# Optimization experiments

Measured on AMD Instinct MI355X. Metric: run time of the kernel, lower is better.

## Reference

```python
import jax, jax.numpy as jnp
import numpy as np

B = 1024          # batch of positions
K = 64            # king squares
F = 640           # 64 squares * 10 piece types
C = 256           # accumulator channels


def setup_inputs() -> dict:
    key = jax.random.key(0)
    k1, k2, k3 = jax.random.split(key, 3)
    piece_positions = jax.random.randint(k1, (B, 64, 10), 0, 2).astype(jnp.bool_)
    king_positions = jax.random.randint(k2, (B, 2), 0, K, dtype=jnp.int32)
    input_weights = jax.random.normal(k3, (K, F + 1, C), dtype=jnp.float32)
    bias = jnp.zeros((C,), dtype=jnp.float32)
    return {
        "piece_positions": piece_positions,
        "king_positions": king_positions,
        "input_weights": input_weights,
        "bias": bias,
    }


def reference(piece_positions, king_positions, input_weights, bias):
    # Flatten the (64, 10) boolean piece plane into 640 HalfKP features.
    b = piece_positions.shape[0]
    p = piece_positions.reshape(b, F).astype(input_weights.dtype)          # (B, 640)
    # Gather each sample's white/black king weight slabs: (B, 2, 641, 256)
    Wg = jnp.take(input_weights, king_positions, axis=0)
    # Sparse-feature sum for both halves, contracted over feature dim and
    # summed over the two king perspectives in one einsum.
    halves = jnp.einsum("bf,bsfc->bc", p, Wg[:, :, :F, :])                 # (B, 256)
    extra = Wg[:, :, F, :].sum(axis=1)                                     # row 640 for each king
    return halves + extra + bias
```

## Files before the change

kernel.cpp:

```cpp
#include <hip/hip_runtime.h>
#include <hip/hip_bf16.h>


#define F_DIM 640
#define C_DIM 256
#define SLAB_STRIDE (641 * 256)
#define NKING 64
#define LCAP 256
#define NC_MAX 64
#define WPAD 17

#define WS_MASK_OFF 0
#define WS_PART_OFF 81920
#define WS_NEED (WS_PART_OFF + 2 * 1024 * 256 * 4)

typedef float  f32x4  __attribute__((ext_vector_type(4)));
typedef short  bf16x8 __attribute__((ext_vector_type(8)));

__device__ __forceinline__ unsigned f2bf_pk(float a, float b) {
    union { float f; unsigned u; } x, y;
    x.f = a; y.f = b;
    const unsigned ra = (x.u + 0x7FFFu + ((x.u >> 16) & 1u)) >> 16;
    const unsigned rb = (y.u + 0x7FFFu + ((y.u >> 16) & 1u)) >> 16;
    return (ra & 0xFFFFu) | (rb << 16);
}

__device__ __forceinline__ bf16x8 mk_a8(unsigned m32, int g) {
    const unsigned by = (m32 >> (g * 8)) & 0xFFu;
    union { unsigned u[4]; bf16x8 v; } r;
    #pragma unroll
    for (int i = 0; i < 4; ++i)
        r.u[i] = (((by >> (2 * i)) & 1u) ? 0x3F80u : 0u) |
                 (((by >> (2 * i + 1)) & 1u) ? 0x3F800000u : 0u);
    return r.v;
}

__global__ __launch_bounds__(256)
void pack_masks(const int* __restrict__ pieces,
                unsigned long long* __restrict__ mask,
                int nwords)
{
    const int gw = blockIdx.x * 4 + (threadIdx.x >> 6);
    const int lane = threadIdx.x & 63;
    if (gw >= nwords) return;
    const int v = pieces[(size_t)gw * 64 + lane];
    const unsigned long long m = __ballot(v != 0);
    if (lane == 0) mask[gw] = m;
}

__global__ __launch_bounds__(512, 8)
void halfkp_mfma(const float* __restrict__ W,
                 const unsigned long long* __restrict__ mask,
                 const int* __restrict__ kings,
                 float* __restrict__ partial,
                 int nent)
{
    const int k  = blockIdx.x;
    const int cq = blockIdx.y;
    const int t  = threadIdx.x;
    const int wv = t >> 6, lane = t & 63;
    const int mt = wv & 1;
    const int kh = wv >> 1;
    const int li = lane & 15, g = lane >> 4;
    const int colG = cq * 16 + li;

    __shared__ unsigned s_W[336 * WPAD];
    __shared__ int s_ent[LCAP];
    __shared__ int s_cb[NC_MAX + 1];
    __shared__ unsigned s_m32[64][21];
    __shared__ f32x4 s_red[4][64];
    __shared__ int s_nk;

    const float* __restrict__ Wq = W + (size_t)k * SLAB_STRIDE + cq * 16;
    float4 ve[3], vo[3];
    #pragma unroll
    for (int it = 0; it < 3; ++it) {
        const int task = t + (it << 9);
        if (task < 336 * 4) {
            const int fp = task >> 2, c4 = task & 3;
            const int fe = min(2 * fp, F_DIM);
            const int fo = min(2 * fp + 1, F_DIM);
            ve[it] = *(const float4*)&Wq[(size_t)fe * C_DIM + c4 * 4];
            vo[it] = *(const float4*)&Wq[(size_t)fo * C_DIM + c4 * 4];
        }
    }

    {
        const int NC = nent >> 6;
        const int nit = NC >> 3;
        unsigned long long mm[8];
        #pragma unroll
        for (int it = 0; it < 8; ++it) {
            if (it < nit) {
                const int c = wv + (it << 3);
                const int kk = kings[(c << 6) + lane];
                mm[it] = __ballot(kk == k);
                if (lane == 0) s_cb[c] = (int)__popcll(mm[it]);
            }
        }
        __syncthreads();
        if (t == 0) {
            int s = 0;
            for (int c = 0; c < NC; ++c) { const int v = s_cb[c]; s_cb[c] = s; s += v; }
            s_nk = min(s, LCAP);
        }
        __syncthreads();
        const unsigned long long lt = (1ull << lane) - 1ull;
        #pragma unroll
        for (int it = 0; it < 8; ++it) {
            if (it < nit) {
                const int c = wv + (it << 3);
                if ((mm[it] >> lane) & 1ull) {
                    const int pos = s_cb[c] + (int)__popcll(mm[it] & lt);
                    if (pos < LCAP) s_ent[pos] = (c << 6) + lane;
                }
            }
        }
    }
    __syncthreads();
    const int n_k = s_nk;

    {
        const int ncc0 = min(n_k, 64);
        for (int idx = t; idx < 64 * 21; idx += 512) {
            const int row = idx & 63, ks = idx >> 6;
            const int id = (row < ncc0) ? s_ent[row] : -1;
            unsigned v = 0;
            if (id >= 0) {
                if (ks < 20) {
                    const unsigned long long mw = mask[(size_t)(id >> 1) * 10 + (ks >> 1)];
                    v = (unsigned)(mw >> ((ks & 1) * 32));
                } else {
                    v = 1u;
                }
            }
            s_m32[row][ks] = v;
        }
    }

    #pragma unroll
    for (int it = 0; it < 3; ++it) {
        const int task = t + (it << 9);
        if (task < 336 * 4) {
            const int fp = task >> 2, c4 = task & 3;
            union { unsigned u[4]; f32x4 v; } pk;
            pk.u[0] = f2bf_pk(ve[it].x, vo[it].x);
            pk.u[1] = f2bf_pk(ve[it].y, vo[it].y);
            pk.u[2] = f2bf_pk(ve[it].z, vo[it].z);
            pk.u[3] = f2bf_pk(ve[it].w, vo[it].w);
            *(f32x4*)&s_W[fp * WPAD + c4 * 4] = pk.v;
        }
    }
    __syncthreads();

    for (int mb = 0; mb < n_k; mb += 64) {
        const int ncc = min(n_k - mb, 64);

        if (mb > 0) {
            __syncthreads();
            for (int idx = t; idx < 64 * 21; idx += 512) {
                const int row = idx & 63, ks = idx >> 6;
                const int id = (row < ncc) ? s_ent[mb + row] : -1;
                unsigned v = 0;
                if (id >= 0) {
                    if (ks < 20) {
                        const unsigned long long mw = mask[(size_t)(id >> 1) * 10 + (ks >> 1)];
                        v = (unsigned)(mw >> ((ks & 1) * 32));
                    } else {
                        v = 1u;
                    }
                }
                s_m32[row][ks] = v;
            }
            __syncthreads();
        }

        const int ntiles = (ncc + 15) >> 4;
        const int ks_beg = (kh == 0) ? 0 : (kh == 1) ? 6 : (kh == 2) ? 11 : 16;
        const int ks_end = (kh == 0) ? 6 : (kh == 1) ? 11 : (kh == 2) ? 16 : 21;

        for (int tb = 0; tb < ntiles; tb += 2) {
            const int tile = tb + mt;
            const bool live = tile * 16 < ncc;
            f32x4 acc = {0.f, 0.f, 0.f, 0.f};
            if (live) {
                const unsigned* mrow = s_m32[tile * 16 + li];
                #pragma unroll 2
                for (int ks = ks_beg; ks < ks_end; ++ks) {
                    const unsigned* bp = &s_W[(ks * 16 + g * 4) * WPAD + li];
                    union { unsigned u[4]; bf16x8 v; } bb;
                    #pragma unroll
                    for (int jj = 0; jj < 4; ++jj)
                        bb.u[jj] = bp[jj * WPAD];
                    const bf16x8 af = mk_a8(mrow[ks], g);
                    acc = __builtin_amdgcn_mfma_f32_16x16x32_bf16(af, bb.v, acc, 0, 0, 0);
                }
                if (kh >= 2) s_red[mt * 2 + kh - 2][lane] = acc;
            }
            __syncthreads();
            if (live && kh < 2) {
                acc += s_red[mt * 2 + kh][lane];
                if (kh == 1) s_red[mt * 2][lane] = acc;
            }
            __syncthreads();
            if (live && kh == 0) {
                acc += s_red[mt * 2][lane];
                #pragma unroll
                for (int i = 0; i < 4; ++i) {
                    const int r = tile * 16 + 4 * g + i;
                    if (r < ncc) {
                        const int id = s_ent[mb + r];
                        partial[(((size_t)(id & 1)) * 1024 + (id >> 1)) * C_DIM + colG] = acc[i];
                    }
                }
            }
            __syncthreads();
        }
    }
}

__global__ __launch_bounds__(256)
void finalize(const float* __restrict__ partial,
              const float* __restrict__ bias,
              float* __restrict__ out)
{
    const int i = blockIdx.x * 256 + threadIdx.x;
    const float4 b4 = ((const float4*)bias)[i & 63];
    const float4 p0 = ((const float4*)partial)[i];
    const float4 p1 = ((const float4*)partial)[1024 * 64 + i];
    float4 o;
    o.x = b4.x + p0.x + p1.x;
    o.y = b4.y + p0.y + p1.y;
    o.z = b4.z + p0.z + p1.z;
    o.w = b4.w + p0.w + p1.w;
    ((float4*)out)[i] = o;
}

__global__ __launch_bounds__(256)
void halfkp_fallback(const int* __restrict__ pieces, const int* __restrict__ kings,
                     const float* __restrict__ W, const float* __restrict__ bias,
                     float* __restrict__ out)
{
    const int b = blockIdx.x;
    const int c = threadIdx.x;
    const int lane = c & 63;
    const int k0 = kings[2 * b + 0];
    const int k1 = kings[2 * b + 1];
    const float* W0 = W + (size_t)k0 * SLAB_STRIDE + c;
    const float* W1 = W + (size_t)k1 * SLAB_STRIDE + c;
    float acc = bias[c] + W0[640 * 256] + W1[640 * 256];
    const int* pi = pieces + (size_t)b * F_DIM;
    #pragma unroll
    for (int ch = 0; ch < 10; ++ch) {
        int v = pi[ch * 64 + lane];
        unsigned long long m = __ballot(v != 0);
        const float* b0 = W0 + ch * 64 * 256;
        const float* b1 = W1 + ch * 64 * 256;
        while (m) {
            const int f = __builtin_ctzll(m);
            m &= m - 1;
            acc += b0[f * 256] + b1[f * 256];
        }
    }
    out[(size_t)b * C_DIM + c] = acc;
}

extern "C" void kernel_launch(void* const* d_in, const int* in_sizes, int n_in,
                              void* d_out, int out_size, void* d_ws, size_t ws_size,
                              hipStream_t stream) {
    const int* pieces = (const int*)d_in[0];
    const int* kings  = (const int*)d_in[1];
    const float* W    = (const float*)d_in[2];
    const float* bias = (const float*)d_in[3];
    float* out        = (float*)d_out;

    const int B = in_sizes[1] / 2;
    const int nent = 2 * B;
    const int nwords = B * 10;

    if (ws_size < (size_t)WS_NEED) {
        halfkp_fallback<<<dim3(B), dim3(C_DIM), 0, stream>>>(pieces, kings, W, bias, out);
        return;
    }

    unsigned long long* mask = (unsigned long long*)((char*)d_ws + WS_MASK_OFF);
    float* part = (float*)((char*)d_ws + WS_PART_OFF);

    pack_masks<<<dim3((nwords + 3) / 4), dim3(256), 0, stream>>>(pieces, mask, nwords);
    halfkp_mfma<<<dim3(NKING, 16), dim3(512), 0, stream>>>(W, mask, kings, part, nent);
    finalize<<<dim3(B * 64 / 256), dim3(256), 0, stream>>>(part, bias, out);
}
```

Before: 27.89 us.

## Split feature dimension into bands per block instead of column quarters

The MFMA kernel now gives each block a 96-row band of the feature dimension across all 256 channels (7 bands per king), instead of a 16-column slice across all 641 rows. Each wave computes four 16-column tiles over three k-steps. This removes the cross-wave reduction through shared memory and its repeated barriers, and lets one A-fragment be reused across four MFMAs. In exchange, per-band partial sums are written to a workspace 7 times larger, and the finalize kernel must read and sum 14 slices. That adds global memory traffic and halves the number of blocks launched.

```diff
diff --git a/kernel.cpp b/kernel.cpp
--- a/kernel.cpp
+++ b/kernel.cpp
@@ -6,13 +6,16 @@
 #define C_DIM 256
 #define SLAB_STRIDE (641 * 256)
 #define NKING 64
+#define NBAND 7
+#define WROWS 96
+#define WPR 48
+#define WSTR 260
 #define LCAP 256
 #define NC_MAX 64
-#define WPAD 17
 
 #define WS_MASK_OFF 0
 #define WS_PART_OFF 81920
-#define WS_NEED (WS_PART_OFF + 2 * 1024 * 256 * 4)
+#define WS_NEED (WS_PART_OFF + NBAND * 2 * 1024 * 256 * 4)
 
 typedef float  f32x4  __attribute__((ext_vector_type(4)));
 typedef short  bf16x8 __attribute__((ext_vector_type(8)));
@@ -48,41 +51,38 @@
     if (lane == 0) mask[gw] = m;
 }
 
-__global__ __launch_bounds__(512, 8)
-void halfkp_mfma(const float* __restrict__ W,
-                 const unsigned long long* __restrict__ mask,
-                 const int* __restrict__ kings,
-                 float* __restrict__ partial,
-                 int nent)
+__global__ __launch_bounds__(512, 4)
+void halfkp_kband(const float* __restrict__ W,
+                  const unsigned long long* __restrict__ mask,
+                  const int* __restrict__ kings,
+                  float* __restrict__ partial,
+                  int nent)
 {
     const int k  = blockIdx.x;
-    const int cq = blockIdx.y;
+    const int bd = blockIdx.y;
     const int t  = threadIdx.x;
     const int wv = t >> 6, lane = t & 63;
     const int mt = wv & 1;
-    const int kh = wv >> 1;
+    const int cg = wv >> 1;
     const int li = lane & 15, g = lane >> 4;
-    const int colG = cq * 16 + li;
-
-    __shared__ unsigned s_W[336 * WPAD];
+
+    __shared__ unsigned s_W[WPR * WSTR];
     __shared__ int s_ent[LCAP];
     __shared__ int s_cb[NC_MAX + 1];
-    __shared__ unsigned s_m32[64][21];
-    __shared__ f32x4 s_red[4][64];
+    __shared__ unsigned s_m32[64][3];
     __shared__ int s_nk;
 
-    const float* __restrict__ Wq = W + (size_t)k * SLAB_STRIDE + cq * 16;
-    float4 ve[3], vo[3];
-    #pragma unroll
-    for (int it = 0; it < 3; ++it) {
+    const int r0 = bd * WROWS;
+    const float* __restrict__ Wk = W + (size_t)k * SLAB_STRIDE;
+    float4 ve[6], vo[6];
+    #pragma unroll
+    for (int it = 0; it < 6; ++it) {
         const int task = t + (it << 9);
-        if (task < 336 * 4) {
-            const int fp = task >> 2, c4 = task & 3;
-            const int fe = min(2 * fp, F_DIM);
-            const int fo = min(2 * fp + 1, F_DIM);
-            ve[it] = *(const float4*)&Wq[(size_t)fe * C_DIM + c4 * 4];
-            vo[it] = *(const float4*)&Wq[(size_t)fo * C_DIM + c4 * 4];
-        }
+        const int pr = task >> 6, c4 = task & 63;
+        const int fe = min(r0 + 2 * pr, F_DIM);
+        const int fo = min(r0 + 2 * pr + 1, F_DIM);
+        ve[it] = *(const float4*)&Wk[(size_t)fe * C_DIM + c4 * 4];
+        vo[it] = *(const float4*)&Wk[(size_t)fo * C_DIM + c4 * 4];
     }
 
     {
@@ -122,34 +122,33 @@
 
     {
         const int ncc0 = min(n_k, 64);
-        for (int idx = t; idx < 64 * 21; idx += 512) {
-            const int row = idx & 63, ks = idx >> 6;
+        for (int idx = t; idx < 64 * 3; idx += 512) {
+            const int row = idx & 63, ksl = idx >> 6;
+            const int ksg = bd * 3 + ksl;
             const int id = (row < ncc0) ? s_ent[row] : -1;
             unsigned v = 0;
             if (id >= 0) {
-                if (ks < 20) {
-                    const unsigned long long mw = mask[(size_t)(id >> 1) * 10 + (ks >> 1)];
-                    v = (unsigned)(mw >> ((ks & 1) * 32));
+                if (ksg < 20) {
+                    const unsigned long long mw = mask[(size_t)(id >> 1) * 10 + (ksg >> 1)];
+                    v = (unsigned)(mw >> ((ksg & 1) * 32));
                 } else {
                     v = 1u;
                 }
             }
-            s_m32[row][ks] = v;
-        }
-    }
-
-    #pragma unroll
-    for (int it = 0; it < 3; ++it) {
+            s_m32[row][ksl] = v;
+        }
+    }
+
+    #pragma unroll
+    for (int it = 0; it < 6; ++it) {
         const int task = t + (it << 9);
-        if (task < 336 * 4) {
-            const int fp = task >> 2, c4 = task & 3;
-            union { unsigned u[4]; f32x4 v; } pk;
-            pk.u[0] = f2bf_pk(ve[it].x, vo[it].x);
-            pk.u[1] = f2bf_pk(ve[it].y, vo[it].y);
-            pk.u[2] = f2bf_pk(ve[it].z, vo[it].z);
-            pk.u[3] = f2bf_pk(ve[it].w, vo[it].w);
-            *(f32x4*)&s_W[fp * WPAD + c4 * 4] = pk.v;
-        }
+        const int pr = task >> 6, c4 = task & 63;
+        union { unsigned u[4]; f32x4 v; } pk;
+        pk.u[0] = f2bf_pk(ve[it].x, vo[it].x);
+        pk.u[1] = f2bf_pk(ve[it].y, vo[it].y);
+        pk.u[2] = f2bf_pk(ve[it].z, vo[it].z);
+        pk.u[3] = f2bf_pk(ve[it].w, vo[it].w);
+        *(f32x4*)&s_W[pr * WSTR + c4 * 4] = pk.v;
     }
     __syncthreads();
 
@@ -158,63 +157,60 @@
 
         if (mb > 0) {
             __syncthreads();
-            for (int idx = t; idx < 64 * 21; idx += 512) {
-                const int row = idx & 63, ks = idx >> 6;
+            for (int idx = t; idx < 64 * 3; idx += 512) {
+                const int row = idx & 63, ksl = idx >> 6;
+                const int ksg = bd * 3 + ksl;
                 const int id = (row < ncc) ? s_ent[mb + row] : -1;
                 unsigned v = 0;
                 if (id >= 0) {
-                    if (ks < 20) {
-                        const unsigned long long mw = mask[(size_t)(id >> 1) * 10 + (ks >> 1)];
-                        v = (unsigned)(mw >> ((ks & 1) * 32));
+                    if (ksg < 20) {
+                        const unsigned long long mw = mask[(size_t)(id >> 1) * 10 + (ksg >> 1)];
+                        v = (unsigned)(mw >> ((ksg & 1) * 32));
                     } else {
                         v = 1u;
                     }
                 }
-                s_m32[row][ks] = v;
+                s_m32[row][ksl] = v;
             }
             __syncthreads();
         }
 
-        const int ntiles = (ncc + 15) >> 4;
-        const int ks_beg = (kh == 0) ? 0 : (kh == 1) ? 6 : (kh == 2) ? 11 : 16;
-        const int ks_end = (kh == 0) ? 6 : (kh == 1) ? 11 : (kh == 2) ? 16 : 21;
-
-        for (int tb = 0; tb < ntiles; tb += 2) {
+        #pragma unroll
+        for (int tb = 0; tb < 4; tb += 2) {
             const int tile = tb + mt;
-            const bool live = tile * 16 < ncc;
-            f32x4 acc = {0.f, 0.f, 0.f, 0.f};
-            if (live) {
+            if (tile * 16 < ncc) {
+                f32x4 acc[4];
+                #pragma unroll
+                for (int nt = 0; nt < 4; ++nt) acc[nt] = (f32x4){0.f, 0.f, 0.f, 0.f};
                 const unsigned* mrow = s_m32[tile * 16 + li];
-                #pragma unroll 2
-                for (int ks = ks_beg; ks < ks_end; ++ks) {
-                    const unsigned* bp = &s_W[(ks * 16 + g * 4) * WPAD + li];
-                    union { unsigned u[4]; bf16x8 v; } bb;
+                #pragma unroll
+                for (int ksl = 0; ksl < 3; ++ksl) {
+                    const bf16x8 af = mk_a8(mrow[ksl], g);
                     #pragma unroll
-                    for (int jj = 0; jj < 4; ++jj)
-                        bb.u[jj] = bp[jj * WPAD];
-                    const bf16x8 af = mk_a8(mrow[ks], g);
-                    acc = __builtin_amdgcn_mfma_f32_16x16x32_bf16(af, bb.v, acc, 0, 0, 0);
-                }
-                if (kh >= 2) s_red[mt * 2 + kh - 2][lane] = acc;
-            }
-            __syncthreads();
-            if (live && kh < 2) {
-                acc += s_red[mt * 2 + kh][lane];
-                if (kh == 1) s_red[mt * 2][lane] = acc;
-            }
-            __syncthreads();
-            if (live && kh == 0) {
-                acc += s_red[mt * 2][lane];
+                    for (int nt = 0; nt < 4; ++nt) {
+                        const unsigned* bp =
+                            &s_W[(ksl * 16 + g * 4) * WSTR + cg * 64 + nt * 16 + li];
+                        union { unsigned u[4]; bf16x8 v; } bb;
+                        bb.u[0] = bp[0];
+                        bb.u[1] = bp[WSTR];
+                        bb.u[2] = bp[2 * WSTR];
+                        bb.u[3] = bp[3 * WSTR];
+                        acc[nt] = __builtin_amdgcn_mfma_f32_16x16x32_bf16(af, bb.v, acc[nt], 0, 0, 0);
+                    }
+                }
                 #pragma unroll
                 for (int i = 0; i < 4; ++i) {
                     const int r = tile * 16 + 4 * g + i;
                     if (r < ncc) {
                         const int id = s_ent[mb + r];
-                        partial[(((size_t)(id & 1)) * 1024 + (id >> 1)) * C_DIM + colG] = acc[i];
+                        float* dst = &partial[(((size_t)(bd * 2 + (id & 1))) * 1024
+                                              + (id >> 1)) * C_DIM + cg * 64];
+                        #pragma unroll
+                        for (int nt = 0; nt < 4; ++nt)
+                            dst[nt * 16 + li] = acc[nt][i];
                     }
                 }
             }
-            __syncthreads();
         }
     }
 }
@@ -225,15 +221,13 @@
               float* __restrict__ out)
 {
     const int i = blockIdx.x * 256 + threadIdx.x;
-    const float4 b4 = ((const float4*)bias)[i & 63];
-    const float4 p0 = ((const float4*)partial)[i];
-    const float4 p1 = ((const float4*)partial)[1024 * 64 + i];
-    float4 o;
-    o.x = b4.x + p0.x + p1.x;
-    o.y = b4.y + p0.y + p1.y;
-    o.z = b4.z + p0.z + p1.z;
-    o.w = b4.w + p0.w + p1.w;
-    ((float4*)out)[i] = o;
+    float4 s = ((const float4*)bias)[i & 63];
+    #pragma unroll
+    for (int sl = 0; sl < NBAND * 2; ++sl) {
+        const float4 p = ((const float4*)partial)[(size_t)sl * 1024 * 64 + i];
+        s.x += p.x; s.y += p.y; s.z += p.z; s.w += p.w;
+    }
+    ((float4*)out)[i] = s;
 }
 
 __global__ __launch_bounds__(256)
@@ -287,6 +281,6 @@
     float* part = (float*)((char*)d_ws + WS_PART_OFF);
 
     pack_masks<<<dim3((nwords + 3) / 4), dim3(256), 0, stream>>>(pieces, mask, nwords);
-    halfkp_mfma<<<dim3(NKING, 16), dim3(512), 0, stream>>>(W, mask, kings, part, nent);
+    halfkp_kband<<<dim3(NKING, NBAND), dim3(512), 0, stream>>>(W, mask, kings, part, nent);
     finalize<<<dim3(B * 64 / 256), dim3(256), 0, stream>>>(part, bias, out);
 }
```

After: 27.87 us. About the same (-0.1%).
